# Optimization experiments

Hardware: AMD Instinct MI355X
Metric: run time of the kernel (lower is better)

Reference implementation:

```python
import jax, jax.numpy as jnp
import numpy as np

VOCAB, D, A = 50000, 200, 32
R, L, B, NNZ = 30000, 40, 10000, 300000


def setup_inputs() -> dict:
    key = jax.random.key(0)
    ks = jax.random.split(key, 12)
    historical_review = jax.random.randint(ks[0], (R, L), 0, VOCAB)
    review_positive = jax.random.normal(ks[1], (R, D), jnp.float32)
    review_negative = jax.random.normal(ks[2], (R, D), jnp.float32)
    u_rows = jax.random.randint(ks[3], (1, NNZ), 0, B)
    u_cols = jax.random.randint(ks[4], (1, NNZ), 0, R)
    user_histor_index = jnp.concatenate([u_rows, u_cols], axis=0)
    user_histor_value = jax.random.uniform(ks[5], (NNZ,), jnp.float32)
    i_rows = jax.random.randint(ks[6], (1, NNZ), 0, B)
    i_cols = jax.random.randint(ks[7], (1, NNZ), 0, R)
    item_histor_index = jnp.concatenate([i_rows, i_cols], axis=0)
    item_histor_value = jax.random.uniform(ks[8], (NNZ,), jnp.float32)
    # parameters (torch nn.Linear convention: y = x @ W.T + b)
    emb_table = jax.random.normal(ks[9], (VOCAB, D), jnp.float32) * 0.1  # frozen
    W_M = jax.random.normal(ks[10], (D, D), jnp.float32) / np.sqrt(D)
    W_W = jax.random.normal(ks[11], (A, D), jnp.float32) / np.sqrt(D)
    b_W = jnp.zeros((A,), jnp.float32)
    return {
        "historical_review": historical_review,
        "review_positive": review_positive,
        "review_negative": review_negative,
        "user_histor_index": user_histor_index,
        "user_histor_value": user_histor_value,
        "item_histor_index": item_histor_index,
        "item_histor_value": item_histor_value,
        "batch_size": B,
        "emb_table": emb_table,
        "W_M": W_M,
        "W_W": W_W,
        "b_W": b_W,
    }


def _spmm(index, value, p_t, n_rows):
    # sparse [n_rows, R] @ p_t [R, A] via gather + segment-sum
    rows, cols = index[0], index[1]
    contrib = value[:, None] * p_t[cols]  # [nnz, A]
    return jax.ops.segment_sum(contrib, rows, num_segments=n_rows)


def reference(historical_review, review_positive, review_negative,
              user_histor_index, user_histor_value,
              item_histor_index, item_histor_value,
              batch_size, emb_table, W_M, W_W, b_W):
    e_w = emb_table[historical_review]                    # [R, L, D] gather
    # dx = matmul(transform_M(e_w), y_s[...,None]) -> [R, L]
    mew = jnp.einsum('rld,ed->rle', e_w, W_M)             # transform_M
    dx = jnp.einsum('rld,rd->rl', mew, review_positive)
    ax = jax.nn.softmax(dx, axis=1)                       # softmax over words
    z_s = jnp.einsum('rld,rl->rd', e_w, ax)               # attention pooling
    p_t = z_s @ W_W.T + b_W                               # [R, A]
    user_aspect = _spmm(user_histor_index, user_histor_value, p_t, batch_size)
    item_aspect = _spmm(item_histor_index, item_histor_value, p_t, batch_size)
    return (user_aspect, item_aspect)
```

## Files before the change

kernel.cpp:

```cpp
#include <hip/hip_runtime.h>
#include <math.h>

#define VOCAB 50000
#define DD 200
#define AA 32
#define RR 30000
#define LL 40
#define BB 10000

typedef _Float16 half2_t __attribute__((ext_vector_type(2)));

static __device__ __forceinline__ unsigned short f2h(float f) {
    return __builtin_bit_cast(unsigned short, (_Float16)f);
}
static __device__ __forceinline__ float hlo(unsigned int u) {
    return (float)__builtin_bit_cast(_Float16, (unsigned short)(u & 0xFFFFu));
}
static __device__ __forceinline__ float hhi(unsigned int u) {
    return (float)__builtin_bit_cast(_Float16, (unsigned short)(u >> 16));
}
static __device__ __forceinline__ unsigned int pkh(float lo, float hi) {
    return (unsigned int)f2h(lo) | ((unsigned int)f2h(hi) << 16);
}
static __device__ __forceinline__ float dot2(unsigned int a, unsigned int b, float acc) {
#if __has_builtin(__builtin_amdgcn_fdot2)
    return __builtin_amdgcn_fdot2(__builtin_bit_cast(half2_t, a),
                                  __builtin_bit_cast(half2_t, b), acc, false);
#else
    return acc + hlo(a) * hlo(b) + hhi(a) * hhi(b);
#endif
}

#define NC4 (VOCAB * DD / 4)
#define NWM ((DD / 2) * DD)
#define NWW (AA * (DD / 2))
__global__ __launch_bounds__(256) void prep_kernel(
    const float* __restrict__ emb, const float* __restrict__ WM,
    const float* __restrict__ WW, unsigned short* __restrict__ emb16,
    unsigned int* __restrict__ WMP, unsigned int* __restrict__ WWP)
{
    int i = blockIdx.x * 256 + threadIdx.x;
    if (i < NC4) {
        float4 f = ((const float4*)emb)[i];
        ushort4 u;
        u.x = f2h(f.x); u.y = f2h(f.y); u.z = f2h(f.z); u.w = f2h(f.w);
        ((ushort4*)emb16)[i] = u;
    } else if (i < NC4 + NWM) {
        int k = i - NC4;
        int e2 = k / DD, d = k - e2 * DD;
        WMP[k] = pkh(WM[(2 * e2) * DD + d], WM[(2 * e2 + 1) * DD + d]);
    } else if (i < NC4 + NWM + NWW) {
        int k = i - NC4 - NWM;
        int a = k / (DD / 2), c = k - a * (DD / 2);
        WWP[k] = pkh(WW[a * DD + 2 * c], WW[a * DD + 2 * c + 1]);
    }
}

__global__ __launch_bounds__(256) void ew_gemm_kernel(
    const unsigned short* __restrict__ emb16, const unsigned int* __restrict__ WWP,
    float* __restrict__ EW)
{
    __shared__ unsigned int et[32][DD / 2];
    __shared__ unsigned int wwT[DD / 2][AA];
    const int r0 = blockIdx.x * 32;
    const int tid = threadIdx.x;

    for (int i = tid; i < AA * (DD / 2); i += 256) {
        int a = i / (DD / 2), c = i - a * (DD / 2);
        wwT[c][a] = WWP[i];
    }
    for (int i = tid; i < 32 * 25; i += 256) {
        int rl = i / 25, c4 = i - rl * 25;
        int r = r0 + rl;
        ((uint4*)et[rl])[c4] = (r < VOCAB)
            ? ((const uint4*)(emb16 + (size_t)r * DD))[c4]
            : make_uint4(0u, 0u, 0u, 0u);
    }
    __syncthreads();

    const int a = tid & 31, rg = tid >> 5;
    #pragma unroll
    for (int k = 0; k < 4; ++k) {
        int rl = rg + 8 * k;
        float acc = 0.f;
        #pragma unroll 4
        for (int c = 0; c < DD / 2; ++c)
            acc = dot2(et[rl][c], wwT[c][a], acc);
        int r = r0 + rl;
        if (r < VOCAB) EW[(size_t)r * AA + a] = acc;
    }
}

__global__ __launch_bounds__(256) void v_gemm_kernel(
    const float* __restrict__ Y, const unsigned int* __restrict__ WMP,
    unsigned int* __restrict__ V16)
{
    __shared__ unsigned int yt[32 * (DD / 2)];
    const int r0 = blockIdx.x * 32;
    const int tid = threadIdx.x;

    for (int i = tid; i < 32 * 50; i += 256) {
        int j = i / 50, c = i - 50 * j;
        int r = r0 + j;
        float4 f = (r < RR) ? ((const float4*)(Y + (size_t)r * DD))[c]
                            : make_float4(0.f, 0.f, 0.f, 0.f);
        uint2 u = make_uint2(pkh(f.x, f.y), pkh(f.z, f.w));
        ((uint2*)yt)[i] = u;
    }
    __syncthreads();

    if (tid < DD) {
        float acc[32];
        #pragma unroll
        for (int j = 0; j < 32; ++j) acc[j] = 0.f;
        for (int e2 = 0; e2 < DD / 2; e2 += 2) {
            unsigned int w0 = WMP[e2 * DD + tid];
            unsigned int w1 = WMP[(e2 + 1) * DD + tid];
            #pragma unroll
            for (int j = 0; j < 32; ++j) {
                uint2 y2 = *(const uint2*)(yt + j * (DD / 2) + e2);
                acc[j] = dot2(y2.x, w0, acc[j]);
                acc[j] = dot2(y2.y, w1, acc[j]);
            }
        }
        #pragma unroll
        for (int j = 0; j < 32; ++j) {
            float partner = __shfl_xor(acc[j], 1);
            int r = r0 + j;
            if (r < RR && (tid & 1) == 0)
                V16[(size_t)r * (DD / 2) + (tid >> 1)] =
                    pkh(acc[j], partner);
        }
    }
}

__global__ __launch_bounds__(256, 8) void attn_kernel(
    const int* __restrict__ hist, const unsigned short* __restrict__ emb16,
    const unsigned int* __restrict__ V16, const float* __restrict__ EW,
    const float* __restrict__ bW, float* __restrict__ PT)
{
    __shared__ __align__(16) unsigned short ew[LL * DD];
    __shared__ __align__(16) unsigned int vp[DD / 2];
    __shared__ float accs[4][AA];
    __shared__ float sws[4];

    const int r = blockIdx.x;
    const int tid = threadIdx.x;
    const int* hrow = hist + r * LL;

    const int i0 = tid, i1 = tid + 256, i2 = tid + 512, i3 = tid + 768;
    const int l0 = i0 / 25, c0 = i0 - 25 * l0;
    const int l1 = i1 / 25, c1 = i1 - 25 * l1;
    const int l2 = i2 / 25, c2 = i2 - 25 * l2;
    const int l3 = i3 / 25, c3 = i3 - 25 * l3;
    const bool has3 = (i3 < LL * 25);

    int w0 = hrow[l0];
    int w1 = hrow[l1];
    int w2 = hrow[l2];
    int w3 = has3 ? hrow[l3] : 0;

    uint4 q0 = ((const uint4*)(emb16 + (size_t)w0 * DD))[c0];
    uint4 q1 = ((const uint4*)(emb16 + (size_t)w1 * DD))[c1];
    uint4 q2 = ((const uint4*)(emb16 + (size_t)w2 * DD))[c2];
    uint4 q3 = has3 ? ((const uint4*)(emb16 + (size_t)w3 * DD))[c3]
                    : make_uint4(0u, 0u, 0u, 0u);
    uint4 vv = make_uint4(0u, 0u, 0u, 0u);
    if (tid < 25) vv = ((const uint4*)(V16 + (size_t)r * (DD / 2)))[tid];

    ((uint4*)ew)[i0] = q0;
    ((uint4*)ew)[i1] = q1;
    ((uint4*)ew)[i2] = q2;
    if (has3) ((uint4*)ew)[i3] = q3;
    if (tid < 25) ((uint4*)vp)[tid] = vv;
    __syncthreads();

    const int wave = tid >> 6, lane = tid & 63;
    const int half = lane >> 5, s = lane & 31;
    const bool act = (s < 25);

    uint4 vq = act ? ((const uint4*)vp)[s] : make_uint4(0u, 0u, 0u, 0u);
    int h = (lane < LL) ? hrow[lane] : 0;

    float pa = 0.f;
    float sw = 0.f;
    #pragma unroll 1
    for (int j = 0; j < 5; ++j) {
        const int l = wave * 10 + 2 * j + half;
        float p = 0.f;
        if (act) {
            uint4 eq = *(const uint4*)(ew + l * DD + s * 8);
            p = dot2(eq.x, vq.x, p);
            p = dot2(eq.y, vq.y, p);
            p = dot2(eq.z, vq.z, p);
            p = dot2(eq.w, vq.w, p);
        }
        #pragma unroll
        for (int off = 16; off; off >>= 1) p += __shfl_xor(p, off);
        float wgt = __expf(p - 8.0f);
        sw += wgt;
        int wi = __shfl(h, l);
        pa += wgt * EW[(size_t)wi * AA + s];
    }

    pa += __shfl_xor(pa, 32);
    float swt = sw + __shfl_xor(sw, 32);
    if (half == 0) accs[wave][s] = pa;
    if (lane == 0) sws[wave] = swt;
    __syncthreads();

    if (tid < AA) {
        float tot = sws[0] + sws[1] + sws[2] + sws[3];
        float t = accs[0][tid] + accs[1][tid] + accs[2][tid] + accs[3][tid];
        PT[r * AA + tid] = t / tot + bW[tid];
    }
}

__global__ __launch_bounds__(256) void spmm_kernel(
    const int* __restrict__ uidx, const float* __restrict__ uval,
    const int* __restrict__ iidx, const float* __restrict__ ival,
    const float* __restrict__ PT, float* __restrict__ out, int nnz)
{
    int g = blockIdx.x * 256 + threadIdx.x;
    int grp = g >> 5;
    int a = g & 31;
    const int gpm = (nnz + 3) >> 2;
    const int* idx = uidx;
    const float* val = uval;
    float* o = out;
    if (grp >= gpm) {
        grp -= gpm;
        if (grp >= gpm) return;
        idx = iidx; val = ival; o += BB * AA;
    }
    const int n0 = grp * 4;

    if (((nnz & 3) == 0) && (n0 + 4 <= nnz)) {
        int4   rows = *(const int4*)(idx + n0);
        int4   cols = *(const int4*)(idx + nnz + n0);
        float4 ws   = *(const float4*)(val + n0);
        atomicAdd(&o[rows.x * AA + a], ws.x * PT[cols.x * AA + a]);
        atomicAdd(&o[rows.y * AA + a], ws.y * PT[cols.y * AA + a]);
        atomicAdd(&o[rows.z * AA + a], ws.z * PT[cols.z * AA + a]);
        atomicAdd(&o[rows.w * AA + a], ws.w * PT[cols.w * AA + a]);
    } else {
        for (int k = 0; k < 4; ++k) {
            int n = n0 + k;
            if (n >= nnz) break;
            int row = idx[n];
            int col = idx[nnz + n];
            float w = val[n];
            atomicAdd(&o[row * AA + a], w * PT[col * AA + a]);
        }
    }
}

extern "C" void kernel_launch(void* const* d_in, const int* in_sizes, int n_in,
                              void* d_out, int out_size, void* d_ws, size_t ws_size,
                              hipStream_t stream) {
    const int*   hist = (const int*)d_in[0];
    const float* ypos = (const float*)d_in[1];
    const int*   uidx = (const int*)d_in[3];
    const float* uval = (const float*)d_in[4];
    const int*   iidx = (const int*)d_in[5];
    const float* ival = (const float*)d_in[6];
    const float* emb  = (const float*)d_in[8];
    const float* WM   = (const float*)d_in[9];
    const float* WW   = (const float*)d_in[10];
    const float* bW   = (const float*)d_in[11];

    unsigned short* emb16 = (unsigned short*)d_ws;
    unsigned int* WMP = (unsigned int*)(emb16 + (size_t)VOCAB * DD);
    unsigned int* WWP = WMP + NWM;
    unsigned int* V16 = WWP + NWW;
    float* PT = (float*)(V16 + (size_t)RR * (DD / 2));
    float* EW = PT + (size_t)RR * AA;
    float* out = (float*)d_out;

    const int nnz = in_sizes[4];

    hipMemsetAsync(d_out, 0, (size_t)out_size * sizeof(float), stream);

    prep_kernel<<<(NC4 + NWM + NWW + 255) / 256, 256, 0, stream>>>(
        emb, WM, WW, emb16, WMP, WWP);
    ew_gemm_kernel<<<(VOCAB + 31) / 32, 256, 0, stream>>>(emb16, WWP, EW);
    v_gemm_kernel<<<(RR + 31) / 32, 256, 0, stream>>>(ypos, WMP, V16);
    attn_kernel<<<RR, 256, 0, stream>>>(hist, emb16, V16, EW, bW, PT);

    const int gpm = (nnz + 3) >> 2;
    const int spmm_blocks = (2 * gpm * 32 + 255) / 256;
    spmm_kernel<<<spmm_blocks, 256, 0, stream>>>(uidx, uval, iidx, ival, PT, out, nnz);
}
```

Measured before the change: 257.5 us.

## Prefetch EW rows into shared memory in attention and rework EW GEMM loop

```diff
diff --git a/kernel.cpp b/kernel.cpp
--- a/kernel.cpp
+++ b/kernel.cpp
@@ -61,14 +61,9 @@
     float* __restrict__ EW)
 {
     __shared__ unsigned int et[32][DD / 2];
-    __shared__ unsigned int wwT[DD / 2][AA];
     const int r0 = blockIdx.x * 32;
     const int tid = threadIdx.x;
 
-    for (int i = tid; i < AA * (DD / 2); i += 256) {
-        int a = i / (DD / 2), c = i - a * (DD / 2);
-        wwT[c][a] = WWP[i];
-    }
     for (int i = tid; i < 32 * 25; i += 256) {
         int rl = i / 25, c4 = i - rl * 25;
         int r = r0 + rl;
@@ -79,16 +74,28 @@
     __syncthreads();
 
     const int a = tid & 31, rg = tid >> 5;
-    #pragma unroll
-    for (int k = 0; k < 4; ++k) {
-        int rl = rg + 8 * k;
-        float acc = 0.f;
-        #pragma unroll 4
-        for (int c = 0; c < DD / 2; ++c)
-            acc = dot2(et[rl][c], wwT[c][a], acc);
-        int r = r0 + rl;
-        if (r < VOCAB) EW[(size_t)r * AA + a] = acc;
-    }
+    const uint4* wp = (const uint4*)(WWP + a * (DD / 2));
+    float acc0 = 0.f, acc1 = 0.f, acc2 = 0.f, acc3 = 0.f;
+    #pragma unroll 1
+    for (int cc = 0; cc < 25; ++cc) {
+        uint4 wq = wp[cc];
+        uint4 e0 = ((const uint4*)et[rg])[cc];
+        uint4 e1 = ((const uint4*)et[rg + 8])[cc];
+        uint4 e2 = ((const uint4*)et[rg + 16])[cc];
+        uint4 e3 = ((const uint4*)et[rg + 24])[cc];
+        acc0 = dot2(e0.x, wq.x, acc0); acc0 = dot2(e0.y, wq.y, acc0);
+        acc0 = dot2(e0.z, wq.z, acc0); acc0 = dot2(e0.w, wq.w, acc0);
+        acc1 = dot2(e1.x, wq.x, acc1); acc1 = dot2(e1.y, wq.y, acc1);
+        acc1 = dot2(e1.z, wq.z, acc1); acc1 = dot2(e1.w, wq.w, acc1);
+        acc2 = dot2(e2.x, wq.x, acc2); acc2 = dot2(e2.y, wq.y, acc2);
+        acc2 = dot2(e2.z, wq.z, acc2); acc2 = dot2(e2.w, wq.w, acc2);
+        acc3 = dot2(e3.x, wq.x, acc3); acc3 = dot2(e3.y, wq.y, acc3);
+        acc3 = dot2(e3.z, wq.z, acc3); acc3 = dot2(e3.w, wq.w, acc3);
+    }
+    if (r0 + rg      < VOCAB) EW[(size_t)(r0 + rg)      * AA + a] = acc0;
+    if (r0 + rg + 8  < VOCAB) EW[(size_t)(r0 + rg + 8)  * AA + a] = acc1;
+    if (r0 + rg + 16 < VOCAB) EW[(size_t)(r0 + rg + 16) * AA + a] = acc2;
+    if (r0 + rg + 24 < VOCAB) EW[(size_t)(r0 + rg + 24) * AA + a] = acc3;
 }
 
 __global__ __launch_bounds__(256) void v_gemm_kernel(
@@ -141,6 +148,7 @@
 {
     __shared__ __align__(16) unsigned short ew[LL * DD];
     __shared__ __align__(16) unsigned int vp[DD / 2];
+    __shared__ float ews[LL * AA];
     __shared__ float accs[4][AA];
     __shared__ float sws[4];
 
@@ -168,11 +176,26 @@
     uint4 vv = make_uint4(0u, 0u, 0u, 0u);
     if (tid < 25) vv = ((const uint4*)(V16 + (size_t)r * (DD / 2)))[tid];
 
+    float g0, g1, g2, g3, g4;
+    {
+        int ia = tid, ib = tid + 256, ic = tid + 512, id = tid + 768, ie = tid + 1024;
+        g0 = EW[(size_t)hrow[ia >> 5] * AA + (ia & 31)];
+        g1 = EW[(size_t)hrow[ib >> 5] * AA + (ib & 31)];
+        g2 = EW[(size_t)hrow[ic >> 5] * AA + (ic & 31)];
+        g3 = EW[(size_t)hrow[id >> 5] * AA + (id & 31)];
+        g4 = EW[(size_t)hrow[ie >> 5] * AA + (ie & 31)];
+    }
+
     ((uint4*)ew)[i0] = q0;
     ((uint4*)ew)[i1] = q1;
     ((uint4*)ew)[i2] = q2;
     if (has3) ((uint4*)ew)[i3] = q3;
     if (tid < 25) ((uint4*)vp)[tid] = vv;
+    ews[tid]        = g0;
+    ews[tid + 256]  = g1;
+    ews[tid + 512]  = g2;
+    ews[tid + 768]  = g3;
+    ews[tid + 1024] = g4;
     __syncthreads();
 
     const int wave = tid >> 6, lane = tid & 63;
@@ -180,7 +203,6 @@
     const bool act = (s < 25);
 
     uint4 vq = act ? ((const uint4*)vp)[s] : make_uint4(0u, 0u, 0u, 0u);
-    int h = (lane < LL) ? hrow[lane] : 0;
 
     float pa = 0.f;
     float sw = 0.f;
@@ -199,8 +221,7 @@
         for (int off = 16; off; off >>= 1) p += __shfl_xor(p, off);
         float wgt = __expf(p - 8.0f);
         sw += wgt;
-        int wi = __shfl(h, l);
-        pa += wgt * EW[(size_t)wi * AA + s];
+        pa += wgt * ews[l * AA + s];
     }
 
     pa += __shfl_xor(pa, 32);
```

Result: faster. 250.7 us (-2.6%).
